# Kernel optimization log

Measured on AMD Instinct MI355X. Metric: run time of the kernel, lower is better.

Reference implementation:

```python
import jax, jax.numpy as jnp
import numpy as np

N = 50000      # nodes
E = 800000     # edges (avg degree 16)
DIN = 256
DOUT = 256
EA = 16        # edge_attr_dim
EH = 32        # edge_mlp_hidden
Z = 0.8        # z_ratio
EPS = 1e-5


def _lin_init(k, fin, fout):
    k1, k2 = jax.random.split(k)
    s = 1.0 / np.sqrt(fin)
    W = jax.random.uniform(k1, (fin, fout), jnp.float32, -s, s)
    b = jax.random.uniform(k2, (fout,), jnp.float32, -s, s)
    return W, b


def setup_inputs() -> dict:
    key = jax.random.key(0)
    ks = jax.random.split(key, 12)
    x = jax.random.normal(ks[0], (N, DIN), dtype=jnp.float32)
    edge_index = jax.random.randint(ks[1], (2, E), 0, N, dtype=jnp.int64)
    edge_weight = jax.random.uniform(ks[2], (E,), dtype=jnp.float32)
    mask = jax.random.bernoulli(ks[3], 0.5, (N, 1))
    edge_attr = jax.random.normal(ks[4], (E, EA), dtype=jnp.float32)
    Wt0, bt0 = _lin_init(ks[5], DIN, DOUT)
    Wt1, bt1 = _lin_init(ks[6], DIN, DOUT)
    Wc0, bc0 = _lin_init(ks[7], DIN + DOUT, DOUT)
    Wc1, bc1 = _lin_init(ks[8], DIN + DOUT, DOUT)
    gn_w = jnp.ones((DOUT,), jnp.float32)
    gn_b = jnp.zeros((DOUT,), jnp.float32)
    gn_alpha = jnp.ones((DOUT,), jnp.float32)  # GraphNorm mean_scale
    Wm1, bm1 = _lin_init(ks[9], EA, EH)
    Wm2, bm2 = _lin_init(ks[10], EH, 1)
    return {
        'x': x, 'edge_index': edge_index, 'edge_weight': edge_weight,
        'mask': mask, 'edge_attr': edge_attr,
        'Wt0': Wt0, 'bt0': bt0, 'Wt1': Wt1, 'bt1': bt1,
        'Wc0': Wc0, 'bc0': bc0, 'Wc1': Wc1, 'bc1': bc1,
        'gn_w': gn_w, 'gn_b': gn_b, 'gn_alpha': gn_alpha,
        'Wm1': Wm1, 'bm1': bm1, 'Wm2': Wm2, 'bm2': bm2,
    }


def _mix(m, a1, a0):
    # torch.where(mask, z*x1 + (1-z)*x0, z*x0 + (1-z)*x1)
    return jnp.where(m, Z * a1 + (1.0 - Z) * a0, Z * a0 + (1.0 - Z) * a1)


def reference(x, edge_index, edge_weight, mask, edge_attr,
              Wt0, bt0, Wt1, bt1, Wc0, bc0, Wc1, bc1,
              gn_w, gn_b, gn_alpha, Wm1, bm1, Wm2, bm2):
    n_node = x.shape[0]
    row, col = edge_index[0], edge_index[1]

    # edge MLP (scalar mode): edge_weight <- softplus(MLP(edge_attr))
    h = jax.nn.relu(edge_attr @ Wm1 + bm1)
    ew = jax.nn.softplus((h @ Wm2 + bm2))[:, 0]  # [E]

    # buildAdj with aggr='mean': row-normalized weights
    deg = jax.ops.segment_sum(ew, row, num_segments=n_node)
    deg = jnp.where(deg < 0.5, deg + 1.0, deg)
    w = ew / deg[row]  # [E]

    # dual-branch transform + masked mix
    x1 = jax.nn.relu(x @ Wt1 + bt1)
    x0 = jax.nn.relu(x @ Wt0 + bt0)
    xm = _mix(mask, x1, x0)  # [N, DOUT]

    # sparse adj @ x : gather at col, scatter-add at row
    agg = jax.ops.segment_sum(w[:, None] * xm[col], row, num_segments=n_node)

    # GraphNorm (single graph): x - alpha*mean, normalize by std
    mean = jnp.mean(agg, axis=0)
    out = agg - gn_alpha * mean
    var = jnp.mean(out * out, axis=0)
    out = gn_w * out * jax.lax.rsqrt(var + EPS) + gn_b

    # dropout inactive in eval mode
    xc = jnp.concatenate([out, x], axis=-1)  # [N, DOUT+DIN]
    c1 = xc @ Wc1 + bc1
    c0 = xc @ Wc0 + bc0
    return _mix(mask, c1, c0)
```

## Files before the change

### kernel.cpp

```cpp
#include <hip/hip_runtime.h>

#define NN 50000
#define NE 800000
#define NNP 50176

typedef __attribute__((ext_vector_type(4))) float f32x4;
typedef __bf16 bf16x8 __attribute__((ext_vector_type(8)));

__device__ __forceinline__ float bfu2f(unsigned short u) {
  return __uint_as_float(((unsigned)u) << 16);
}
__device__ __forceinline__ unsigned short f2bf(float f) {
  unsigned u = __float_as_uint(f);
  u += 0x7fffu + ((u >> 16) & 1u);
  return (unsigned short)(u >> 16);
}

__device__ __forceinline__ void gload16(const void* g, void* l) {
  __builtin_amdgcn_global_load_lds(
      (const __attribute__((address_space(1))) unsigned int*)g,
      (__attribute__((address_space(3))) unsigned int*)l, 16, 0, 0);
}

__global__ __launch_bounds__(256) void prep_kernel(
    const float* __restrict__ X, unsigned short* __restrict__ xbf,
    const int* __restrict__ ei, int* __restrict__ cnt, int* __restrict__ rank,
    const float* __restrict__ Wt1, const float* __restrict__ Wt0,
    const float* __restrict__ Wc1, const float* __restrict__ Wc0,
    unsigned short* __restrict__ WTt1, unsigned short* __restrict__ WTt0,
    unsigned short* __restrict__ WTc1, unsigned short* __restrict__ WTc0) {
  __shared__ unsigned short T[32 * 40];
  const int bid = blockIdx.x;
  const int t = threadIdx.x;
  if (bid < 3125) {
    const int e = bid * 256 + t;
    if (e < NE) rank[e] = atomicAdd(&cnt[ei[e]], 1);
    return;
  }
  if (bid < 3125 + 6272) {
    const int gid = (bid - 3125) * 256 + t;
    const long base = (long)gid * 8;
    const int row = (int)(base >> 8);
    unsigned short o[8];
    if (row < NN) {
      f32x4 a = *(const f32x4*)(X + base);
      f32x4 b = *(const f32x4*)(X + base + 4);
#pragma unroll
      for (int i = 0; i < 4; i++) { o[i] = f2bf(a[i]); o[4 + i] = f2bf(b[i]); }
    } else {
#pragma unroll
      for (int i = 0; i < 8; i++) o[i] = 0;
    }
    *(uint4*)(xbf + base) = *(const uint4*)o;
    return;
  }
  int tb = bid - (3125 + 6272);
  const float* W;
  unsigned short* WT;
  int K, kx, ny;
  if (tb < 64) { W = Wt1; WT = WTt1; K = 256; kx = tb & 7; ny = tb >> 3; }
  else if (tb < 128) { tb -= 64; W = Wt0; WT = WTt0; K = 256; kx = tb & 7; ny = tb >> 3; }
  else if (tb < 256) { tb -= 128; W = Wc1; WT = WTc1; K = 512; kx = tb & 15; ny = tb >> 4; }
  else { tb -= 256; W = Wc0; WT = WTc0; K = 512; kx = tb & 15; ny = tb >> 4; }
  const int k0 = kx * 32, n0 = ny * 32;
  const int kk = t >> 3, nn = (t & 7) * 4;
  f32x4 v = *(const f32x4*)(W + (k0 + kk) * 256 + n0 + nn);
#pragma unroll
  for (int i = 0; i < 4; i++) T[(nn + i) * 40 + kk] = f2bf(v[i]);
  __syncthreads();
  const int nn2 = t >> 3, kk2 = (t & 7) * 4;
  unsigned short o[4];
#pragma unroll
  for (int i = 0; i < 4; i++) o[i] = T[nn2 * 40 + kk2 + i];
  *(uint2*)(WT + (n0 + nn2) * K + k0 + kk2) = *(const uint2*)o;
}

__global__ __launch_bounds__(256) void scan1_kernel(const int* __restrict__ cnt,
                                                    int* __restrict__ blockSum) {
  __shared__ int sd[256];
  const int t = threadIdx.x;
  sd[t] = cnt[blockIdx.x * 256 + t];
  __syncthreads();
  for (int off = 128; off > 0; off >>= 1) {
    if (t < off) sd[t] += sd[t + off];
    __syncthreads();
  }
  if (t == 0) blockSum[blockIdx.x] = sd[0];
}

__global__ __launch_bounds__(256) void scan2_kernel(int* __restrict__ blockSum) {
  __shared__ int sd[256];
  const int t = threadIdx.x;
  int v = (t < 196) ? blockSum[t] : 0;
  sd[t] = v;
  __syncthreads();
  for (int off = 1; off < 256; off <<= 1) {
    int y = (t >= off) ? sd[t - off] : 0;
    __syncthreads();
    sd[t] += y;
    __syncthreads();
  }
  int ex = (t == 0) ? 0 : sd[t - 1];
  __syncthreads();
  if (t < 196) blockSum[t] = ex;
}

__global__ __launch_bounds__(256) void scan3_kernel(
    const int* __restrict__ cnt, const int* __restrict__ blockSum,
    int* __restrict__ start) {
  __shared__ int sd[256];
  const int t = threadIdx.x;
  const int row = blockIdx.x * 256 + t;
  const int c = cnt[row];
  sd[t] = c;
  __syncthreads();
  for (int off = 1; off < 256; off <<= 1) {
    int y = (t >= off) ? sd[t - off] : 0;
    __syncthreads();
    sd[t] += y;
    __syncthreads();
  }
  start[row] = blockSum[blockIdx.x] + sd[t] - c;
}

__device__ __forceinline__ void mlp4(float a0, float a1, float a2, float a3,
                                     const f32x4* __restrict__ w,
                                     f32x4& h0, f32x4& h1, f32x4& h2, f32x4& h3,
                                     f32x4& h4, f32x4& h5, f32x4& h6, f32x4& h7) {
  h0 += w[0] * a0;  h1 += w[1] * a0;  h2 += w[2] * a0;  h3 += w[3] * a0;
  h4 += w[4] * a0;  h5 += w[5] * a0;  h6 += w[6] * a0;  h7 += w[7] * a0;
  h0 += w[8] * a1;  h1 += w[9] * a1;  h2 += w[10] * a1; h3 += w[11] * a1;
  h4 += w[12] * a1; h5 += w[13] * a1; h6 += w[14] * a1; h7 += w[15] * a1;
  h0 += w[16] * a2; h1 += w[17] * a2; h2 += w[18] * a2; h3 += w[19] * a2;
  h4 += w[20] * a2; h5 += w[21] * a2; h6 += w[22] * a2; h7 += w[23] * a2;
  h0 += w[24] * a3; h1 += w[25] * a3; h2 += w[26] * a3; h3 += w[27] * a3;
  h4 += w[28] * a3; h5 += w[29] * a3; h6 += w[30] * a3; h7 += w[31] * a3;
}

__device__ __forceinline__ float rdot(f32x4 h, f32x4 w) {
  float s = fmaxf(h[0], 0.0f) * w[0];
  s = fmaf(fmaxf(h[1], 0.0f), w[1], s);
  s = fmaf(fmaxf(h[2], 0.0f), w[2], s);
  s = fmaf(fmaxf(h[3], 0.0f), w[3], s);
  return s;
}

__global__ __launch_bounds__(256) void mlp_fill_kernel(
    const float* __restrict__ ea,
    const float* __restrict__ Wm1, const float* __restrict__ bm1,
    const float* __restrict__ Wm2, const float* __restrict__ bm2,
    const int* __restrict__ ei, const int* __restrict__ start,
    const int* __restrict__ rank, uint2* __restrict__ colw) {
  __shared__ __align__(16) float w1[512];
  __shared__ __align__(16) float b1[32];
  __shared__ __align__(16) float w2[32];
  __shared__ float b2s[1];
  const int t = threadIdx.x;
  w1[t] = Wm1[t];
  w1[t + 256] = Wm1[t + 256];
  if (t < 32) { b1[t] = bm1[t]; w2[t] = Wm2[t]; }
  if (t == 0) b2s[0] = bm2[0];
  __syncthreads();
  const int e = blockIdx.x * 256 + t;
  if (e >= NE) return;
  f32x4 r0 = *(const f32x4*)(ea + e * 16);
  f32x4 r1 = *(const f32x4*)(ea + e * 16 + 4);
  f32x4 r2 = *(const f32x4*)(ea + e * 16 + 8);
  f32x4 r3 = *(const f32x4*)(ea + e * 16 + 12);
  const f32x4* bv = (const f32x4*)b1;
  f32x4 h0 = bv[0], h1 = bv[1], h2 = bv[2], h3 = bv[3];
  f32x4 h4 = bv[4], h5 = bv[5], h6 = bv[6], h7 = bv[7];
  const f32x4* wv = (const f32x4*)w1;
  mlp4(r0[0], r0[1], r0[2], r0[3], wv, h0, h1, h2, h3, h4, h5, h6, h7);
  mlp4(r1[0], r1[1], r1[2], r1[3], wv + 32, h0, h1, h2, h3, h4, h5, h6, h7);
  mlp4(r2[0], r2[1], r2[2], r2[3], wv + 64, h0, h1, h2, h3, h4, h5, h6, h7);
  mlp4(r3[0], r3[1], r3[2], r3[3], wv + 96, h0, h1, h2, h3, h4, h5, h6, h7);
  const f32x4* w2v = (const f32x4*)w2;
  float s = b2s[0];
  s += rdot(h0, w2v[0]) + rdot(h1, w2v[1]) + rdot(h2, w2v[2]) + rdot(h3, w2v[3]);
  s += rdot(h4, w2v[4]) + rdot(h5, w2v[5]) + rdot(h6, w2v[6]) + rdot(h7, w2v[7]);
  const float sp = (s > 0.0f) ? (s + log1pf(expf(-s))) : log1pf(expf(s));
  uint2 p;
  p.x = (unsigned)ei[NE + e];
  p.y = __float_as_uint(sp);
  colw[start[ei[e]] + rank[e]] = p;
}

template <int KTOT, bool SPLIT, bool OUT_BF16>
__global__ __launch_bounds__(256, 3) void gemm_dual(
    const unsigned short* __restrict__ A0, const unsigned short* __restrict__ A1,
    const unsigned short* __restrict__ WT1, const unsigned short* __restrict__ WT0,
    const float* __restrict__ bias1, const float* __restrict__ bias0,
    const int* __restrict__ mask, void* __restrict__ outp) {
  __shared__ __align__(16) unsigned short Al[128 * 64];
  __shared__ __align__(16) unsigned short B1l[64 * 64];
  __shared__ __align__(16) unsigned short B0l[64 * 64];
  const int t = threadIdx.x;
  const int bid = blockIdx.y * gridDim.x + blockIdx.x;
  const int swz = (bid & 7) * 196 + (bid >> 3);
  const int bx = swz & 3, by = swz >> 2;
  const int row0 = by * 128, col0 = bx * 64;
  const int wv = t >> 6, lane = t & 63, m = lane & 15, q = lane >> 4;
  const int wr = wv >> 1, wc = wv & 1;
  const int arow = t >> 3, ach = t & 7;
  f32x4 acc1[4][2], acc0[4][2];
#pragma unroll
  for (int rf = 0; rf < 4; rf++)
#pragma unroll
    for (int nt = 0; nt < 2; nt++) { acc1[rf][nt] = (f32x4)(0.0f); acc0[rf][nt] = (f32x4)(0.0f); }

  for (int k0 = 0; k0 < KTOT; k0 += 64) {
    const unsigned short* Ab;
    int kr;
    if constexpr (SPLIT) {
      if (k0 < 256) { Ab = A0; kr = k0; } else { Ab = A1; kr = k0 - 256; }
    } else { Ab = A0; kr = k0; }
#pragma unroll
    for (int i = 0; i < 4; i++) {
      const int r = arow + i * 32;
      gload16(Ab + (size_t)(row0 + r) * 256 + kr + ((ach ^ (r & 7)) << 3),
              &Al[(i * 256 + t) * 8]);
    }
#pragma unroll
    for (int i = 0; i < 2; i++) {
      const int r = arow + i * 32;
      const int sc = (ach ^ (r & 7)) << 3;
      gload16(WT1 + (size_t)(col0 + r) * KTOT + k0 + sc, &B1l[(i * 256 + t) * 8]);
      gload16(WT0 + (size_t)(col0 + r) * KTOT + k0 + sc, &B0l[(i * 256 + t) * 8]);
    }
    __syncthreads();
#pragma unroll
    for (int kk = 0; kk < 2; kk++) {
      bf16x8 af[4];
#pragma unroll
      for (int rf = 0; rf < 4; rf++) {
        const int r = wr * 64 + rf * 16 + m;
        af[rf] = *(const bf16x8*)&Al[r * 64 + (((kk * 4 + q) ^ (r & 7)) << 3)];
      }
#pragma unroll
      for (int nt = 0; nt < 2; nt++) {
        const int n = wc * 32 + nt * 16 + m;
        const int off = n * 64 + (((kk * 4 + q) ^ (n & 7)) << 3);
        bf16x8 f1 = *(const bf16x8*)&B1l[off];
        bf16x8 f0 = *(const bf16x8*)&B0l[off];
#pragma unroll
        for (int rf = 0; rf < 4; rf++) {
          acc1[rf][nt] = __builtin_amdgcn_mfma_f32_16x16x32_bf16(af[rf], f1, acc1[rf][nt], 0, 0, 0);
          acc0[rf][nt] = __builtin_amdgcn_mfma_f32_16x16x32_bf16(af[rf], f0, acc0[rf][nt], 0, 0, 0);
        }
      }
    }
    __syncthreads();
  }

#pragma unroll
  for (int rf = 0; rf < 4; rf++) {
    const int rbase = row0 + wr * 64 + rf * 16 + q * 4;
    int mk[4];
#pragma unroll
    for (int r = 0; r < 4; r++) mk[r] = (rbase + r < NN) ? mask[rbase + r] : 0;
#pragma unroll
    for (int nt = 0; nt < 2; nt++) {
      const int gc = col0 + wc * 32 + nt * 16 + m;
      const float bb1 = bias1[gc];
      const float bb0 = bias0[gc];
#pragma unroll
      for (int r = 0; r < 4; r++) {
        const int grr = rbase + r;
        if (grr < NN) {
          float v1 = acc1[rf][nt][r] + bb1;
          float v0 = acc0[rf][nt][r] + bb0;
          if constexpr (OUT_BF16) {
            v1 = fmaxf(v1, 0.0f);
            v0 = fmaxf(v0, 0.0f);
            float o = mk[r] ? (0.8f * v1 + 0.2f * v0) : (0.8f * v0 + 0.2f * v1);
            ((unsigned short*)outp)[(size_t)grr * 256 + gc] = f2bf(o);
          } else {
            float o = mk[r] ? (0.8f * v1 + 0.2f * v0) : (0.8f * v0 + 0.2f * v1);
            ((float*)outp)[(size_t)grr * 256 + gc] = o;
          }
        }
      }
    }
  }
}

#define EDGE(u, wgt) do { \
  dsum += wgt; \
  acc[0] = fmaf(wgt, __uint_as_float(u.x << 16), acc[0]); \
  acc[1] = fmaf(wgt, __uint_as_float(u.x & 0xffff0000u), acc[1]); \
  acc[2] = fmaf(wgt, __uint_as_float(u.y << 16), acc[2]); \
  acc[3] = fmaf(wgt, __uint_as_float(u.y & 0xffff0000u), acc[3]); \
} while (0)

__global__ __launch_bounds__(256) void aggregate_kernel(
    const int* __restrict__ start, const int* __restrict__ cnt,
    const uint2* __restrict__ colw,
    const unsigned short* __restrict__ xmb, unsigned short* __restrict__ aggb) {
  const int wave = threadIdx.x >> 6, lane = threadIdx.x & 63;
  const int row = blockIdx.x * 4 + wave;
  const int s = start[row];
  const int c = cnt[row];
  const int choff = lane * 4;
  f32x4 acc = (f32x4)(0.0f);
  float dsum = 0.0f;
  int i = 0;
  for (; i + 8 <= c; i += 8) {
    uint2 cw0 = colw[s + i],     cw1 = colw[s + i + 1];
    uint2 cw2 = colw[s + i + 2], cw3 = colw[s + i + 3];
    uint2 cw4 = colw[s + i + 4], cw5 = colw[s + i + 5];
    uint2 cw6 = colw[s + i + 6], cw7 = colw[s + i + 7];
    uint2 u0 = *(const uint2*)(xmb + (size_t)cw0.x * 256 + choff);
    uint2 u1 = *(const uint2*)(xmb + (size_t)cw1.x * 256 + choff);
    uint2 u2 = *(const uint2*)(xmb + (size_t)cw2.x * 256 + choff);
    uint2 u3 = *(const uint2*)(xmb + (size_t)cw3.x * 256 + choff);
    uint2 u4 = *(const uint2*)(xmb + (size_t)cw4.x * 256 + choff);
    uint2 u5 = *(const uint2*)(xmb + (size_t)cw5.x * 256 + choff);
    uint2 u6 = *(const uint2*)(xmb + (size_t)cw6.x * 256 + choff);
    uint2 u7 = *(const uint2*)(xmb + (size_t)cw7.x * 256 + choff);
    EDGE(u0, __uint_as_float(cw0.y));
    EDGE(u1, __uint_as_float(cw1.y));
    EDGE(u2, __uint_as_float(cw2.y));
    EDGE(u3, __uint_as_float(cw3.y));
    EDGE(u4, __uint_as_float(cw4.y));
    EDGE(u5, __uint_as_float(cw5.y));
    EDGE(u6, __uint_as_float(cw6.y));
    EDGE(u7, __uint_as_float(cw7.y));
  }
  for (; i + 4 <= c; i += 4) {
    uint2 cw0 = colw[s + i],     cw1 = colw[s + i + 1];
    uint2 cw2 = colw[s + i + 2], cw3 = colw[s + i + 3];
    uint2 u0 = *(const uint2*)(xmb + (size_t)cw0.x * 256 + choff);
    uint2 u1 = *(const uint2*)(xmb + (size_t)cw1.x * 256 + choff);
    uint2 u2 = *(const uint2*)(xmb + (size_t)cw2.x * 256 + choff);
    uint2 u3 = *(const uint2*)(xmb + (size_t)cw3.x * 256 + choff);
    EDGE(u0, __uint_as_float(cw0.y));
    EDGE(u1, __uint_as_float(cw1.y));
    EDGE(u2, __uint_as_float(cw2.y));
    EDGE(u3, __uint_as_float(cw3.y));
  }
  for (; i < c; i++) {
    uint2 cw0 = colw[s + i];
    uint2 u0 = *(const uint2*)(xmb + (size_t)cw0.x * 256 + choff);
    EDGE(u0, __uint_as_float(cw0.y));
  }
  float d = (dsum < 0.5f) ? dsum + 1.0f : dsum;
  const float inv = 1.0f / d;
  unsigned short o[4];
#pragma unroll
  for (int j = 0; j < 4; j++) o[j] = f2bf(acc[j] * inv);
  *(uint2*)(aggb + (size_t)row * 256 + choff) = *(const uint2*)o;
}

__global__ __launch_bounds__(256) void stats_kernel(
    const unsigned short* __restrict__ aggb, float* __restrict__ S1, float* __restrict__ S2) {
  const int c = threadIdx.x;
  const int r0 = blockIdx.x * 200;
  float s1 = 0.0f, s2 = 0.0f;
  for (int r = 0; r < 200; r++) {
    float v = bfu2f(aggb[(r0 + r) * 256 + c]);
    s1 += v;
    s2 = fmaf(v, v, s2);
  }
  unsafeAtomicAdd(&S1[c], s1);
  unsafeAtomicAdd(&S2[c], s2);
}

__global__ __launch_bounds__(256) void norm_agg_kernel(
    const unsigned short* __restrict__ aggb,
    const float* __restrict__ S1, const float* __restrict__ S2,
    const float* __restrict__ gw, const float* __restrict__ gb,
    const float* __restrict__ ga, unsigned short* __restrict__ aggn) {
  __shared__ float scL[256];
  __shared__ float shL[256];
  const int t = threadIdx.x;
  {
    const float inv_n = 1.0f / (float)NN;
    float mean = S1[t] * inv_n;
    float ex2 = S2[t] * inv_n;
    float am = ga[t] * mean;
    float var = ex2 - 2.0f * am * mean + am * am;
    float sc = gw[t] * rsqrtf(var + 1e-5f);
    scL[t] = sc;
    shL[t] = gb[t] - sc * am;
  }
  __syncthreads();
  const int gid = blockIdx.x * 256 + t;
  const long base = (long)gid * 8;
  const int row = (int)(base >> 8);
  const int c = (int)(base & 255);
  unsigned short o[8];
  if (row < NN) {
    uint4 u = *(const uint4*)(aggb + base);
    const unsigned short* us = (const unsigned short*)&u;
#pragma unroll
    for (int i = 0; i < 8; i++) o[i] = f2bf(fmaf(scL[c + i], bfu2f(us[i]), shL[c + i]));
  } else {
#pragma unroll
    for (int i = 0; i < 8; i++) o[i] = 0;
  }
  *(uint4*)(aggn + base) = *(const uint4*)o;
}

extern "C" void kernel_launch(void* const* d_in, const int* in_sizes, int n_in,
                              void* d_out, int out_size, void* d_ws, size_t ws_size,
                              hipStream_t stream) {
  (void)in_sizes; (void)n_in; (void)out_size; (void)ws_size;
  const float* x   = (const float*)d_in[0];
  const int*   ei  = (const int*)d_in[1];
  const int*   msk = (const int*)d_in[3];
  const float* ea  = (const float*)d_in[4];
  const float* Wt0 = (const float*)d_in[5];
  const float* bt0 = (const float*)d_in[6];
  const float* Wt1 = (const float*)d_in[7];
  const float* bt1 = (const float*)d_in[8];
  const float* Wc0 = (const float*)d_in[9];
  const float* bc0 = (const float*)d_in[10];
  const float* Wc1 = (const float*)d_in[11];
  const float* bc1 = (const float*)d_in[12];
  const float* gnw = (const float*)d_in[13];
  const float* gnb = (const float*)d_in[14];
  const float* gna = (const float*)d_in[15];
  const float* Wm1 = (const float*)d_in[16];
  const float* bm1 = (const float*)d_in[17];
  const float* Wm2 = (const float*)d_in[18];
  const float* bm2 = (const float*)d_in[19];

  char* ws = (char*)d_ws;
  int* cnt      = (int*)ws;
  int* startA   = (int*)(ws + 200704);
  int* blockSum = (int*)(ws + 401408);
  float* S1     = (float*)(ws + 402432);
  float* S2     = (float*)(ws + 403456);
  unsigned short* WTt1 = (unsigned short*)(ws + 404480);
  unsigned short* WTt0 = (unsigned short*)(ws + 535552);
  unsigned short* WTc1 = (unsigned short*)(ws + 666624);
  unsigned short* WTc0 = (unsigned short*)(ws + 928768);
  int* rankA    = (int*)(ws + 1190912);
  uint2* colw   = (uint2*)(ws + 4390912);
  unsigned short* xmb  = (unsigned short*)(ws + 10790912);
  unsigned short* aggb = (unsigned short*)(ws + 36481024);
  unsigned short* xbf  = (unsigned short*)(ws + 62171136);

  hipMemsetAsync(ws, 0, 404480, stream);

  prep_kernel<<<9781, 256, 0, stream>>>(x, xbf, ei, cnt, rankA,
                                        Wt1, Wt0, Wc1, Wc0,
                                        WTt1, WTt0, WTc1, WTc0);
  scan1_kernel<<<196, 256, 0, stream>>>(cnt, blockSum);
  scan2_kernel<<<1, 256, 0, stream>>>(blockSum);
  scan3_kernel<<<196, 256, 0, stream>>>(cnt, blockSum, startA);
  mlp_fill_kernel<<<3125, 256, 0, stream>>>(ea, Wm1, bm1, Wm2, bm2, ei, startA, rankA, colw);

  gemm_dual<256, false, true><<<dim3(4, 392), 256, 0, stream>>>(
      xbf, (const unsigned short*)nullptr, WTt1, WTt0, bt1, bt0, msk, xmb);

  aggregate_kernel<<<12500, 256, 0, stream>>>(startA, cnt, colw, xmb, aggb);
  stats_kernel<<<250, 256, 0, stream>>>(aggb, S1, S2);
  norm_agg_kernel<<<6272, 256, 0, stream>>>(aggb, S1, S2, gnw, gnb, gna, xmb );

  gemm_dual<512, true, false><<<dim3(4, 392), 256, 0, stream>>>(
      xmb , xbf, WTc1, WTc0, bc1, bc0, msk, d_out);
}
```

Before: 393.1 us.

## Fold GraphNorm into combine weights, fuse stats into aggregate, merge GEMM with edge MLP

The per-column GraphNorm statistics are now accumulated inside the aggregate kernel, which removes the separate stats pass. The normalization is folded into the combine GEMM by scaling the transposed bf16 weights and adjusting the biases, so the norm_agg pass over the aggregated features goes away. The first dual GEMM and the edge-MLP fill now run as one launch with a block-index split, and scan2/scan3 are merged, which cuts launches and extra memory traffic. Costs: the folded weights are rounded to bf16 twice, and the aggregate kernel gains 512 atomics per block plus a __syncthreads. The bias-fold buffers reuse the xmb region, and the padding rows of aggb are now zeroed in prep.

```diff
diff --git a/kernel.cpp b/kernel.cpp
--- a/kernel.cpp
+++ b/kernel.cpp
@@ -3,6 +3,22 @@
 #define NN 50000
 #define NE 800000
 #define NNP 50176
+
+#define OFF_START 200704
+#define OFF_BSUM  401408
+#define OFF_S1    402432
+#define OFF_S2    403456
+#define OFF_WTT1  404480
+#define OFF_WTT0  535552
+#define OFF_WTC1  666624
+#define OFF_WTC0  928768
+#define OFF_RANK  1190912
+#define OFF_COLW  4390912
+#define OFF_XMB   10790912
+#define OFF_AGG   36481024
+#define OFF_XBF   62171136
+#define OFF_B1F   10790912
+#define OFF_B0F   10791936
 
 typedef __attribute__((ext_vector_type(4))) float f32x4;
 typedef __bf16 bf16x8 __attribute__((ext_vector_type(8)));
@@ -28,7 +44,8 @@
     const float* __restrict__ Wt1, const float* __restrict__ Wt0,
     const float* __restrict__ Wc1, const float* __restrict__ Wc0,
     unsigned short* __restrict__ WTt1, unsigned short* __restrict__ WTt0,
-    unsigned short* __restrict__ WTc1, unsigned short* __restrict__ WTc0) {
+    unsigned short* __restrict__ WTc1, unsigned short* __restrict__ WTc0,
+    unsigned short* __restrict__ aggb) {
   __shared__ unsigned short T[32 * 40];
   const int bid = blockIdx.x;
   const int t = threadIdx.x;
@@ -54,25 +71,30 @@
     *(uint4*)(xbf + base) = *(const uint4*)o;
     return;
   }
-  int tb = bid - (3125 + 6272);
-  const float* W;
-  unsigned short* WT;
-  int K, kx, ny;
-  if (tb < 64) { W = Wt1; WT = WTt1; K = 256; kx = tb & 7; ny = tb >> 3; }
-  else if (tb < 128) { tb -= 64; W = Wt0; WT = WTt0; K = 256; kx = tb & 7; ny = tb >> 3; }
-  else if (tb < 256) { tb -= 128; W = Wc1; WT = WTc1; K = 512; kx = tb & 15; ny = tb >> 4; }
-  else { tb -= 256; W = Wc0; WT = WTc0; K = 512; kx = tb & 15; ny = tb >> 4; }
-  const int k0 = kx * 32, n0 = ny * 32;
-  const int kk = t >> 3, nn = (t & 7) * 4;
-  f32x4 v = *(const f32x4*)(W + (k0 + kk) * 256 + n0 + nn);
-#pragma unroll
-  for (int i = 0; i < 4; i++) T[(nn + i) * 40 + kk] = f2bf(v[i]);
-  __syncthreads();
-  const int nn2 = t >> 3, kk2 = (t & 7) * 4;
-  unsigned short o[4];
-#pragma unroll
-  for (int i = 0; i < 4; i++) o[i] = T[nn2 * 40 + kk2 + i];
-  *(uint2*)(WT + (n0 + nn2) * K + k0 + kk2) = *(const uint2*)o;
+  if (bid < 3125 + 6272 + 384) {
+    int tb = bid - (3125 + 6272);
+    const float* W;
+    unsigned short* WT;
+    int K, kx, ny;
+    if (tb < 64) { W = Wt1; WT = WTt1; K = 256; kx = tb & 7; ny = tb >> 3; }
+    else if (tb < 128) { tb -= 64; W = Wt0; WT = WTt0; K = 256; kx = tb & 7; ny = tb >> 3; }
+    else if (tb < 256) { tb -= 128; W = Wc1; WT = WTc1; K = 512; kx = tb & 15; ny = tb >> 4; }
+    else { tb -= 256; W = Wc0; WT = WTc0; K = 512; kx = tb & 15; ny = tb >> 4; }
+    const int k0 = kx * 32, n0 = ny * 32;
+    const int kk = t >> 3, nn = (t & 7) * 4;
+    f32x4 v = *(const f32x4*)(W + (k0 + kk) * 256 + n0 + nn);
+#pragma unroll
+    for (int i = 0; i < 4; i++) T[(nn + i) * 40 + kk] = f2bf(v[i]);
+    __syncthreads();
+    const int nn2 = t >> 3, kk2 = (t & 7) * 4;
+    unsigned short o[4];
+#pragma unroll
+    for (int i = 0; i < 4; i++) o[i] = T[nn2 * 40 + kk2 + i];
+    *(uint2*)(WT + (n0 + nn2) * K + k0 + kk2) = *(const uint2*)o;
+    return;
+  }
+  const int idx = (bid - (3125 + 6272 + 384)) * 256 + t;
+  if (idx < 5632) ((uint4*)(aggb + (size_t)NN * 256))[idx] = make_uint4(0, 0, 0, 0);
 }
 
 __global__ __launch_bounds__(256) void scan1_kernel(const int* __restrict__ cnt,
@@ -88,29 +110,25 @@
   if (t == 0) blockSum[blockIdx.x] = sd[0];
 }
 
-__global__ __launch_bounds__(256) void scan2_kernel(int* __restrict__ blockSum) {
-  __shared__ int sd[256];
-  const int t = threadIdx.x;
-  int v = (t < 196) ? blockSum[t] : 0;
-  sd[t] = v;
-  __syncthreads();
-  for (int off = 1; off < 256; off <<= 1) {
-    int y = (t >= off) ? sd[t - off] : 0;
-    __syncthreads();
-    sd[t] += y;
-    __syncthreads();
-  }
-  int ex = (t == 0) ? 0 : sd[t - 1];
-  __syncthreads();
-  if (t < 196) blockSum[t] = ex;
-}
-
-__global__ __launch_bounds__(256) void scan3_kernel(
+__global__ __launch_bounds__(256) void scan23_kernel(
     const int* __restrict__ cnt, const int* __restrict__ blockSum,
     int* __restrict__ start) {
   __shared__ int sd[256];
-  const int t = threadIdx.x;
-  const int row = blockIdx.x * 256 + t;
+  __shared__ int pfx;
+  const int t = threadIdx.x;
+  const int bid = blockIdx.x;
+  int v = (t < 196) ? blockSum[t] : 0;
+  sd[t] = v;
+  __syncthreads();
+  for (int off = 1; off < 256; off <<= 1) {
+    int y = (t >= off) ? sd[t - off] : 0;
+    __syncthreads();
+    sd[t] += y;
+    __syncthreads();
+  }
+  if (t == 0) pfx = (bid == 0) ? 0 : sd[bid - 1];
+  __syncthreads();
+  const int row = bid * 256 + t;
   const int c = cnt[row];
   sd[t] = c;
   __syncthreads();
@@ -120,7 +138,7 @@
     sd[t] += y;
     __syncthreads();
   }
-  start[row] = blockSum[blockIdx.x] + sd[t] - c;
+  start[row] = pfx + sd[t] - c;
 }
 
 __device__ __forceinline__ void mlp4(float a0, float a1, float a2, float a3,
@@ -145,23 +163,132 @@
   return s;
 }
 
-__global__ __launch_bounds__(256) void mlp_fill_kernel(
+template <int KTOT, bool SPLIT, bool OUT_BF16>
+__device__ __forceinline__ void gemm_tile(unsigned short* SH, int task,
+    const unsigned short* __restrict__ A0, const unsigned short* __restrict__ A1,
+    const unsigned short* __restrict__ WT1, const unsigned short* __restrict__ WT0,
+    const float* __restrict__ bias1, const float* __restrict__ bias0,
+    const int* __restrict__ mask, void* __restrict__ outp) {
+  unsigned short* Al  = SH;
+  unsigned short* B1l = SH + 8192;
+  unsigned short* B0l = SH + 12288;
+  const int t = threadIdx.x;
+  const int swz = (task & 7) * 196 + (task >> 3);
+  const int bx = swz & 3, by = swz >> 2;
+  const int row0 = by * 128, col0 = bx * 64;
+  const int wv = t >> 6, lane = t & 63, m = lane & 15, q = lane >> 4;
+  const int wr = wv >> 1, wc = wv & 1;
+  const int arow = t >> 3, ach = t & 7;
+  f32x4 acc1[4][2], acc0[4][2];
+#pragma unroll
+  for (int rf = 0; rf < 4; rf++)
+#pragma unroll
+    for (int nt = 0; nt < 2; nt++) { acc1[rf][nt] = (f32x4)(0.0f); acc0[rf][nt] = (f32x4)(0.0f); }
+
+  for (int k0 = 0; k0 < KTOT; k0 += 64) {
+    const unsigned short* Ab;
+    int kr;
+    if constexpr (SPLIT) {
+      if (k0 < 256) { Ab = A0; kr = k0; } else { Ab = A1; kr = k0 - 256; }
+    } else { Ab = A0; kr = k0; }
+#pragma unroll
+    for (int i = 0; i < 4; i++) {
+      const int r = arow + i * 32;
+      gload16(Ab + (size_t)(row0 + r) * 256 + kr + ((ach ^ (r & 7)) << 3),
+              &Al[(i * 256 + t) * 8]);
+    }
+#pragma unroll
+    for (int i = 0; i < 2; i++) {
+      const int r = arow + i * 32;
+      const int sc = (ach ^ (r & 7)) << 3;
+      gload16(WT1 + (size_t)(col0 + r) * KTOT + k0 + sc, &B1l[(i * 256 + t) * 8]);
+      gload16(WT0 + (size_t)(col0 + r) * KTOT + k0 + sc, &B0l[(i * 256 + t) * 8]);
+    }
+    __syncthreads();
+#pragma unroll
+    for (int kk = 0; kk < 2; kk++) {
+      bf16x8 af[4];
+#pragma unroll
+      for (int rf = 0; rf < 4; rf++) {
+        const int r = wr * 64 + rf * 16 + m;
+        af[rf] = *(const bf16x8*)&Al[r * 64 + (((kk * 4 + q) ^ (r & 7)) << 3)];
+      }
+#pragma unroll
+      for (int nt = 0; nt < 2; nt++) {
+        const int n = wc * 32 + nt * 16 + m;
+        const int off = n * 64 + (((kk * 4 + q) ^ (n & 7)) << 3);
+        bf16x8 f1 = *(const bf16x8*)&B1l[off];
+        bf16x8 f0 = *(const bf16x8*)&B0l[off];
+#pragma unroll
+        for (int rf = 0; rf < 4; rf++) {
+          acc1[rf][nt] = __builtin_amdgcn_mfma_f32_16x16x32_bf16(af[rf], f1, acc1[rf][nt], 0, 0, 0);
+          acc0[rf][nt] = __builtin_amdgcn_mfma_f32_16x16x32_bf16(af[rf], f0, acc0[rf][nt], 0, 0, 0);
+        }
+      }
+    }
+    __syncthreads();
+  }
+
+#pragma unroll
+  for (int rf = 0; rf < 4; rf++) {
+    const int rbase = row0 + wr * 64 + rf * 16 + q * 4;
+    int mk[4];
+#pragma unroll
+    for (int r = 0; r < 4; r++) mk[r] = (rbase + r < NN) ? mask[rbase + r] : 0;
+#pragma unroll
+    for (int nt = 0; nt < 2; nt++) {
+      const int gc = col0 + wc * 32 + nt * 16 + m;
+      const float bb1 = bias1[gc];
+      const float bb0 = bias0[gc];
+#pragma unroll
+      for (int r = 0; r < 4; r++) {
+        const int grr = rbase + r;
+        if (grr < NN) {
+          float v1 = acc1[rf][nt][r] + bb1;
+          float v0 = acc0[rf][nt][r] + bb0;
+          if constexpr (OUT_BF16) {
+            v1 = fmaxf(v1, 0.0f);
+            v0 = fmaxf(v0, 0.0f);
+            float o = mk[r] ? (0.8f * v1 + 0.2f * v0) : (0.8f * v0 + 0.2f * v1);
+            ((unsigned short*)outp)[(size_t)grr * 256 + gc] = f2bf(o);
+          } else {
+            float o = mk[r] ? (0.8f * v1 + 0.2f * v0) : (0.8f * v0 + 0.2f * v1);
+            ((float*)outp)[(size_t)grr * 256 + gc] = o;
+          }
+        }
+      }
+    }
+  }
+}
+
+__global__ __launch_bounds__(256, 3) void midk(
+    const unsigned short* __restrict__ xbf,
+    const unsigned short* __restrict__ WTt1, const unsigned short* __restrict__ WTt0,
+    const float* __restrict__ bt1, const float* __restrict__ bt0,
+    const int* __restrict__ msk, unsigned short* __restrict__ xmb,
     const float* __restrict__ ea,
     const float* __restrict__ Wm1, const float* __restrict__ bm1,
     const float* __restrict__ Wm2, const float* __restrict__ bm2,
     const int* __restrict__ ei, const int* __restrict__ start,
     const int* __restrict__ rank, uint2* __restrict__ colw) {
-  __shared__ __align__(16) float w1[512];
-  __shared__ __align__(16) float b1[32];
-  __shared__ __align__(16) float w2[32];
-  __shared__ float b2s[1];
-  const int t = threadIdx.x;
+  __shared__ __align__(16) unsigned short SH[128 * 64 + 64 * 64 + 64 * 64];
+  const int bid = blockIdx.x;
+  const int t = threadIdx.x;
+  if (bid < 1568) {
+    gemm_tile<256, false, true>(SH, bid, xbf, (const unsigned short*)nullptr,
+                                WTt1, WTt0, bt1, bt0, msk, xmb);
+    return;
+  }
+  float* w1 = (float*)SH;
+  float* b1 = w1 + 512;
+  float* w2 = b1 + 32;
+  float* b2s = w2 + 32;
   w1[t] = Wm1[t];
   w1[t + 256] = Wm1[t + 256];
   if (t < 32) { b1[t] = bm1[t]; w2[t] = Wm2[t]; }
   if (t == 0) b2s[0] = bm2[0];
   __syncthreads();
-  const int e = blockIdx.x * 256 + t;
+  const int e = (bid - 1568) * 256 + t;
   if (e >= NE) return;
   f32x4 r0 = *(const f32x4*)(ea + e * 16);
   f32x4 r1 = *(const f32x4*)(ea + e * 16 + 4);
@@ -186,103 +313,14 @@
   colw[start[ei[e]] + rank[e]] = p;
 }
 
-template <int KTOT, bool SPLIT, bool OUT_BF16>
-__global__ __launch_bounds__(256, 3) void gemm_dual(
-    const unsigned short* __restrict__ A0, const unsigned short* __restrict__ A1,
+__global__ __launch_bounds__(256, 3) void gemm_combine(
+    const unsigned short* __restrict__ aggb, const unsigned short* __restrict__ xbf,
     const unsigned short* __restrict__ WT1, const unsigned short* __restrict__ WT0,
     const float* __restrict__ bias1, const float* __restrict__ bias0,
-    const int* __restrict__ mask, void* __restrict__ outp) {
-  __shared__ __align__(16) unsigned short Al[128 * 64];
-  __shared__ __align__(16) unsigned short B1l[64 * 64];
-  __shared__ __align__(16) unsigned short B0l[64 * 64];
-  const int t = threadIdx.x;
-  const int bid = blockIdx.y * gridDim.x + blockIdx.x;
-  const int swz = (bid & 7) * 196 + (bid >> 3);
-  const int bx = swz & 3, by = swz >> 2;
-  const int row0 = by * 128, col0 = bx * 64;
-  const int wv = t >> 6, lane = t & 63, m = lane & 15, q = lane >> 4;
-  const int wr = wv >> 1, wc = wv & 1;
-  const int arow = t >> 3, ach = t & 7;
-  f32x4 acc1[4][2], acc0[4][2];
-#pragma unroll
-  for (int rf = 0; rf < 4; rf++)
-#pragma unroll
-    for (int nt = 0; nt < 2; nt++) { acc1[rf][nt] = (f32x4)(0.0f); acc0[rf][nt] = (f32x4)(0.0f); }
-
-  for (int k0 = 0; k0 < KTOT; k0 += 64) {
-    const unsigned short* Ab;
-    int kr;
-    if constexpr (SPLIT) {
-      if (k0 < 256) { Ab = A0; kr = k0; } else { Ab = A1; kr = k0 - 256; }
-    } else { Ab = A0; kr = k0; }
-#pragma unroll
-    for (int i = 0; i < 4; i++) {
-      const int r = arow + i * 32;
-      gload16(Ab + (size_t)(row0 + r) * 256 + kr + ((ach ^ (r & 7)) << 3),
-              &Al[(i * 256 + t) * 8]);
-    }
-#pragma unroll
-    for (int i = 0; i < 2; i++) {
-      const int r = arow + i * 32;
-      const int sc = (ach ^ (r & 7)) << 3;
-      gload16(WT1 + (size_t)(col0 + r) * KTOT + k0 + sc, &B1l[(i * 256 + t) * 8]);
-      gload16(WT0 + (size_t)(col0 + r) * KTOT + k0 + sc, &B0l[(i * 256 + t) * 8]);
-    }
-    __syncthreads();
-#pragma unroll
-    for (int kk = 0; kk < 2; kk++) {
-      bf16x8 af[4];
-#pragma unroll
-      for (int rf = 0; rf < 4; rf++) {
-        const int r = wr * 64 + rf * 16 + m;
-        af[rf] = *(const bf16x8*)&Al[r * 64 + (((kk * 4 + q) ^ (r & 7)) << 3)];
-      }
-#pragma unroll
-      for (int nt = 0; nt < 2; nt++) {
-        const int n = wc * 32 + nt * 16 + m;
-        const int off = n * 64 + (((kk * 4 + q) ^ (n & 7)) << 3);
-        bf16x8 f1 = *(const bf16x8*)&B1l[off];
-        bf16x8 f0 = *(const bf16x8*)&B0l[off];
-#pragma unroll
-        for (int rf = 0; rf < 4; rf++) {
-          acc1[rf][nt] = __builtin_amdgcn_mfma_f32_16x16x32_bf16(af[rf], f1, acc1[rf][nt], 0, 0, 0);
-          acc0[rf][nt] = __builtin_amdgcn_mfma_f32_16x16x32_bf16(af[rf], f0, acc0[rf][nt], 0, 0, 0);
-        }
-      }
-    }
-    __syncthreads();
-  }
-
-#pragma unroll
-  for (int rf = 0; rf < 4; rf++) {
-    const int rbase = row0 + wr * 64 + rf * 16 + q * 4;
-    int mk[4];
-#pragma unroll
-    for (int r = 0; r < 4; r++) mk[r] = (rbase + r < NN) ? mask[rbase + r] : 0;
-#pragma unroll
-    for (int nt = 0; nt < 2; nt++) {
-      const int gc = col0 + wc * 32 + nt * 16 + m;
-      const float bb1 = bias1[gc];
-      const float bb0 = bias0[gc];
-#pragma unroll
-      for (int r = 0; r < 4; r++) {
-        const int grr = rbase + r;
-        if (grr < NN) {
-          float v1 = acc1[rf][nt][r] + bb1;
-          float v0 = acc0[rf][nt][r] + bb0;
-          if constexpr (OUT_BF16) {
-            v1 = fmaxf(v1, 0.0f);
-            v0 = fmaxf(v0, 0.0f);
-            float o = mk[r] ? (0.8f * v1 + 0.2f * v0) : (0.8f * v0 + 0.2f * v1);
-            ((unsigned short*)outp)[(size_t)grr * 256 + gc] = f2bf(o);
-          } else {
-            float o = mk[r] ? (0.8f * v1 + 0.2f * v0) : (0.8f * v0 + 0.2f * v1);
-            ((float*)outp)[(size_t)grr * 256 + gc] = o;
-          }
-        }
-      }
-    }
-  }
+    const int* __restrict__ mask, float* __restrict__ out) {
+  __shared__ __align__(16) unsigned short SH[128 * 64 + 64 * 64 + 64 * 64];
+  const int task = blockIdx.y * gridDim.x + blockIdx.x;
+  gemm_tile<512, true, false>(SH, task, aggb, xbf, WT1, WT0, bias1, bias0, mask, out);
 }
 
 #define EDGE(u, wgt) do { \
@@ -296,7 +334,10 @@
 __global__ __launch_bounds__(256) void aggregate_kernel(
     const int* __restrict__ start, const int* __restrict__ cnt,
     const uint2* __restrict__ colw,
-    const unsigned short* __restrict__ xmb, unsigned short* __restrict__ aggb) {
+    const unsigned short* __restrict__ xmb, unsigned short* __restrict__ aggb,
+    float* __restrict__ S1, float* __restrict__ S2) {
+  __shared__ float s1L[4][256];
+  __shared__ float s2L[4][256];
   const int wave = threadIdx.x >> 6, lane = threadIdx.x & 63;
   const int row = blockIdx.x * 4 + wave;
   const int s = start[row];
@@ -346,60 +387,57 @@
   }
   float d = (dsum < 0.5f) ? dsum + 1.0f : dsum;
   const float inv = 1.0f / d;
+  f32x4 v;
   unsigned short o[4];
 #pragma unroll
-  for (int j = 0; j < 4; j++) o[j] = f2bf(acc[j] * inv);
+  for (int j = 0; j < 4; j++) { v[j] = acc[j] * inv; o[j] = f2bf(v[j]); }
   *(uint2*)(aggb + (size_t)row * 256 + choff) = *(const uint2*)o;
-}
-
-__global__ __launch_bounds__(256) void stats_kernel(
-    const unsigned short* __restrict__ aggb, float* __restrict__ S1, float* __restrict__ S2) {
-  const int c = threadIdx.x;
-  const int r0 = blockIdx.x * 200;
-  float s1 = 0.0f, s2 = 0.0f;
-  for (int r = 0; r < 200; r++) {
-    float v = bfu2f(aggb[(r0 + r) * 256 + c]);
-    s1 += v;
-    s2 = fmaf(v, v, s2);
-  }
-  unsafeAtomicAdd(&S1[c], s1);
-  unsafeAtomicAdd(&S2[c], s2);
-}
-
-__global__ __launch_bounds__(256) void norm_agg_kernel(
-    const unsigned short* __restrict__ aggb,
+  *(f32x4*)&s1L[wave][choff] = v;
+  f32x4 v2;
+#pragma unroll
+  for (int j = 0; j < 4; j++) v2[j] = v[j] * v[j];
+  *(f32x4*)&s2L[wave][choff] = v2;
+  __syncthreads();
+  const int t = threadIdx.x;
+  const float p1 = s1L[0][t] + s1L[1][t] + s1L[2][t] + s1L[3][t];
+  const float p2 = s2L[0][t] + s2L[1][t] + s2L[2][t] + s2L[3][t];
+  unsafeAtomicAdd(&S1[t], p1);
+  unsafeAtomicAdd(&S2[t], p2);
+}
+
+__global__ __launch_bounds__(256) void fold_kernel(
     const float* __restrict__ S1, const float* __restrict__ S2,
-    const float* __restrict__ gw, const float* __restrict__ gb,
-    const float* __restrict__ ga, unsigned short* __restrict__ aggn) {
-  __shared__ float scL[256];
-  __shared__ float shL[256];
-  const int t = threadIdx.x;
-  {
-    const float inv_n = 1.0f / (float)NN;
-    float mean = S1[t] * inv_n;
-    float ex2 = S2[t] * inv_n;
-    float am = ga[t] * mean;
-    float var = ex2 - 2.0f * am * mean + am * am;
-    float sc = gw[t] * rsqrtf(var + 1e-5f);
-    scL[t] = sc;
-    shL[t] = gb[t] - sc * am;
-  }
-  __syncthreads();
-  const int gid = blockIdx.x * 256 + t;
-  const long base = (long)gid * 8;
-  const int row = (int)(base >> 8);
-  const int c = (int)(base & 255);
-  unsigned short o[8];
-  if (row < NN) {
-    uint4 u = *(const uint4*)(aggb + base);
-    const unsigned short* us = (const unsigned short*)&u;
-#pragma unroll
-    for (int i = 0; i < 8; i++) o[i] = f2bf(fmaf(scL[c + i], bfu2f(us[i]), shL[c + i]));
-  } else {
-#pragma unroll
-    for (int i = 0; i < 8; i++) o[i] = 0;
-  }
-  *(uint4*)(aggn + base) = *(const uint4*)o;
+    const float* __restrict__ gnw, const float* __restrict__ gnb,
+    const float* __restrict__ gna,
+    const float* __restrict__ Wc1, const float* __restrict__ Wc0,
+    const float* __restrict__ bc1, const float* __restrict__ bc0,
+    unsigned short* __restrict__ WTc1, unsigned short* __restrict__ WTc0,
+    float* __restrict__ b1f, float* __restrict__ b0f) {
+  __shared__ float r1[256];
+  __shared__ float r0[256];
+  const int n = blockIdx.x, t = threadIdx.x;
+  const float inv_n = 1.0f / (float)NN;
+  const float mean = S1[t] * inv_n;
+  const float ex2 = S2[t] * inv_n;
+  const float am = gna[t] * mean;
+  const float var = ex2 - 2.0f * am * mean + am * am;
+  const float sc = gnw[t] * rsqrtf(var + 1e-5f);
+  const float sh = gnb[t] - sc * am;
+  const float w1 = bfu2f(WTc1[n * 512 + t]);
+  WTc1[n * 512 + t] = f2bf(w1 * sc);
+  const float w0 = bfu2f(WTc0[n * 512 + t]);
+  WTc0[n * 512 + t] = f2bf(w0 * sc);
+  r1[t] = sh * Wc1[t * 256 + n];
+  r0[t] = sh * Wc0[t * 256 + n];
+  __syncthreads();
+  for (int off = 128; off > 0; off >>= 1) {
+    if (t < off) { r1[t] += r1[t + off]; r0[t] += r0[t + off]; }
+    __syncthreads();
+  }
+  if (t == 0) {
+    b1f[n] = bc1[n] + r1[0];
+    b0f[n] = bc0[n] + r0[0];
+  }
 }
 
 extern "C" void kernel_launch(void* const* d_in, const int* in_sizes, int n_in,
@@ -428,37 +466,34 @@
 
   char* ws = (char*)d_ws;
   int* cnt      = (int*)ws;
-  int* startA   = (int*)(ws + 200704);
-  int* blockSum = (int*)(ws + 401408);
-  float* S1     = (float*)(ws + 402432);
-  float* S2     = (float*)(ws + 403456);
-  unsigned short* WTt1 = (unsigned short*)(ws + 404480);
-  unsigned short* WTt0 = (unsigned short*)(ws + 535552);
-  unsigned short* WTc1 = (unsigned short*)(ws + 666624);
-  unsigned short* WTc0 = (unsigned short*)(ws + 928768);
-  int* rankA    = (int*)(ws + 1190912);
-  uint2* colw   = (uint2*)(ws + 4390912);
-  unsigned short* xmb  = (unsigned short*)(ws + 10790912);
-  unsigned short* aggb = (unsigned short*)(ws + 36481024);
-  unsigned short* xbf  = (unsigned short*)(ws + 62171136);
+  int* startA   = (int*)(ws + OFF_START);
+  int* blockSum = (int*)(ws + OFF_BSUM);
+  float* S1     = (float*)(ws + OFF_S1);
+  float* S2     = (float*)(ws + OFF_S2);
+  unsigned short* WTt1 = (unsigned short*)(ws + OFF_WTT1);
+  unsigned short* WTt0 = (unsigned short*)(ws + OFF_WTT0);
+  unsigned short* WTc1 = (unsigned short*)(ws + OFF_WTC1);
+  unsigned short* WTc0 = (unsigned short*)(ws + OFF_WTC0);
+  int* rankA    = (int*)(ws + OFF_RANK);
+  uint2* colw   = (uint2*)(ws + OFF_COLW);
+  unsigned short* xmb  = (unsigned short*)(ws + OFF_XMB);
+  unsigned short* aggb = (unsigned short*)(ws + OFF_AGG);
+  unsigned short* xbf  = (unsigned short*)(ws + OFF_XBF);
+  float* b1f = (float*)(ws + OFF_B1F);
+  float* b0f = (float*)(ws + OFF_B0F);
 
   hipMemsetAsync(ws, 0, 404480, stream);
 
-  prep_kernel<<<9781, 256, 0, stream>>>(x, xbf, ei, cnt, rankA,
+  prep_kernel<<<9803, 256, 0, stream>>>(x, xbf, ei, cnt, rankA,
                                         Wt1, Wt0, Wc1, Wc0,
-                                        WTt1, WTt0, WTc1, WTc0);
+                                        WTt1, WTt0, WTc1, WTc0, aggb);
   scan1_kernel<<<196, 256, 0, stream>>>(cnt, blockSum);
-  scan2_kernel<<<1, 256, 0, stream>>>(blockSum);
-  scan3_kernel<<<196, 256, 0, stream>>>(cnt, blockSum, startA);
-  mlp_fill_kernel<<<3125, 256, 0, stream>>>(ea, Wm1, bm1, Wm2, bm2, ei, startA, rankA, colw);
-
-  gemm_dual<256, false, true><<<dim3(4, 392), 256, 0, stream>>>(
-      xbf, (const unsigned short*)nullptr, WTt1, WTt0, bt1, bt0, msk, xmb);
-
-  aggregate_kernel<<<12500, 256, 0, stream>>>(startA, cnt, colw, xmb, aggb);
-  stats_kernel<<<250, 256, 0, stream>>>(aggb, S1, S2);
-  norm_agg_kernel<<<6272, 256, 0, stream>>>(aggb, S1, S2, gnw, gnb, gna, xmb );
-
-  gemm_dual<512, true, false><<<dim3(4, 392), 256, 0, stream>>>(
-      xmb , xbf, WTc1, WTc0, bc1, bc0, msk, d_out);
-}
+  scan23_kernel<<<196, 256, 0, stream>>>(cnt, blockSum, startA);
+  midk<<<4693, 256, 0, stream>>>(xbf, WTt1, WTt0, bt1, bt0, msk, xmb,
+                                 ea, Wm1, bm1, Wm2, bm2, ei, startA, rankA, colw);
+  aggregate_kernel<<<12500, 256, 0, stream>>>(startA, cnt, colw, xmb, aggb, S1, S2);
+  fold_kernel<<<256, 256, 0, stream>>>(S1, S2, gnw, gnb, gna, Wc1, Wc0, bc1, bc0,
+                                       WTc1, WTc0, b1f, b0f);
+  gemm_combine<<<dim3(4, 392), 256, 0, stream>>>(aggb, xbf, WTc1, WTc0, b1f, b0f,
+                                                 msk, (float*)d_out);
+}
```

Measured after the change: 613.4 us. 1.56x slower.
